# Kernel optimization log

Hardware: AMD Instinct MI355X
Metric: run time of the kernel (lower is better)

Reference implementation:

```python
import jax, jax.numpy as jnp
import numpy as np

D_DYN = 256    # dynamic_dim
D_STAT = 64    # static_dim
U_DIM = 48     # config.model.u_dim
N_OBS = 80     # num_prod*2 + num_inj = 32*2 + 16
T = 128        # rollout steps
B = 2048       # batch


def setup_inputs() -> dict:
    key = jax.random.key(0)
    k = jax.random.split(key, 8)
    z_dyn = jax.random.normal(k[0], (B, D_DYN), dtype=jnp.float32)
    z_static = jax.random.normal(k[1], (B, D_STAT), dtype=jnp.float32)
    dt = jnp.ones((1,), dtype=jnp.float32) * 0.05
    U = jax.random.normal(k[2], (T, B, U_DIM), dtype=jnp.float32)
    # learned params, initialized as in the torch module
    eig_raw = jnp.zeros((D_DYN,), dtype=jnp.float32)
    V = jnp.eye(D_DYN, dtype=jnp.float32) + jax.random.normal(k[3], (D_DYN, D_DYN), dtype=jnp.float32) * 0.01
    L = jax.random.normal(k[4], (D_DYN, U_DIM), dtype=jnp.float32) * (1.0 / np.sqrt(U_DIM))
    C = jax.random.normal(k[5], (N_OBS, D_DYN), dtype=jnp.float32) * (1.0 / np.sqrt(D_DYN))
    Dm = jax.random.normal(k[6], (N_OBS, U_DIM), dtype=jnp.float32) * (1.0 / np.sqrt(U_DIM))
    return {"z_dyn": z_dyn, "z_static": z_static, "dt": dt, "U": U,
            "eig_raw": eig_raw, "V": V, "L": L, "C": C, "Dm": Dm}


def reference(z_dyn, z_static, dt, U, eig_raw, V, L, C, Dm):
    # Stable Koopman operator: K = V diag(sigmoid(eig_raw)*0.99) V^{-1}
    eigvals = jax.nn.sigmoid(eig_raw) * 0.99
    K = (V * eigvals[None, :]) @ jnp.linalg.inv(V)  # [d, d]
    KT, LT, CT, DT = K.T, L.T, C.T, Dm.T
    dts = dt[0]

    def step(z, ut):
        ut_dt = ut * dts                 # [B, u_dim]
        z = z @ KT + ut_dt @ LT          # [B, d]
        y = z @ CT + ut_dt @ DT          # [B, n_obs]
        return z, (z, y)

    _, (Z, Y) = jax.lax.scan(step, z_dyn, U)
    return Z, Y  # [T, B, d], [T, B, n_obs]
```

## Files before the change

kernel.cpp:

```cpp
#include <hip/hip_runtime.h>

#define D_   256
#define UD_  48
#define NO_  80
#define T_   128
#define B_   2048

typedef __bf16 bf16x8 __attribute__((ext_vector_type(8)));
typedef float  f32x4  __attribute__((ext_vector_type(4)));
typedef unsigned short ushort_t;

static __device__ __forceinline__ ushort_t f2bf(float f){
  return __builtin_bit_cast(ushort_t, (__bf16)f);
}
static __device__ __forceinline__ float bf2f(ushort_t u){
  union { unsigned int i; float f; } c; c.i = ((unsigned int)u) << 16; return c.f;
}
static __device__ __forceinline__ f32x4 mfma16(bf16x8 a, bf16x8 b, f32x4 c){
  return __builtin_amdgcn_mfma_f32_16x16x32_bf16(a, b, c, 0, 0, 0);
}


__global__ void __launch_bounds__(256) k_pre(
    const float* __restrict__ V, const float* __restrict__ eig,
    const float* __restrict__ Cmat,
    float* __restrict__ W, float* __restrict__ Cw,
    float* __restrict__ lam, float* __restrict__ dVd){
  const int bid = blockIdx.x, tid = threadIdx.x;
  if (bid < 256){
    const float* Ar = V + bid*D_;
    float a0=0.f,a1=0.f,a2=0.f,a3=0.f;
    #pragma unroll 4
    for (int k = 0; k < D_; k += 4){
      a0 += Ar[k+0] * V[(k+0)*D_ + tid];
      a1 += Ar[k+1] * V[(k+1)*D_ + tid];
      a2 += Ar[k+2] * V[(k+2)*D_ + tid];
      a3 += Ar[k+3] * V[(k+3)*D_ + tid];
    }
    W[bid*D_ + tid] = (a0+a1)+(a2+a3);
  } else if (bid < 256 + NO_){
    const int n = bid - 256;
    float acc = 0.f;
    #pragma unroll 4
    for (int j = 0; j < D_; ++j) acc += Cmat[n*D_ + j] * V[j*D_ + tid];
    Cw[n*D_ + tid] = acc;
  } else {
    lam[tid] = 0.99f / (1.0f + expf(-eig[tid]));
    const float v = V[tid*D_ + tid];
    dVd[tid] = v - bf2f(f2bf(v));
  }
}

__global__ void __launch_bounds__(256) k_x1(
    const float* __restrict__ V, const float* __restrict__ W,
    float* __restrict__ X1){
  const int i = blockIdx.x, j = threadIdx.x;
  const float* Ar = V + i*D_;
  float a0=0.f,a1=0.f,a2=0.f,a3=0.f;
  #pragma unroll 4
  for (int k = 0; k < D_; k += 4){
    a0 += Ar[k+0] * W[(k+0)*D_ + j];
    a1 += Ar[k+1] * W[(k+1)*D_ + j];
    a2 += Ar[k+2] * W[(k+2)*D_ + j];
    a3 += Ar[k+3] * W[(k+3)*D_ + j];
  }
  X1[i*D_ + j] = (i == j ? 4.0f : 0.0f) - 6.0f*V[i*D_ + j] + 4.0f*W[i*D_ + j]
                 - ((a0+a1)+(a2+a3));
}

__global__ void __launch_bounds__(256) k_mm_mul(
    const float* __restrict__ A, const float* __restrict__ B,
    float* __restrict__ Cm){
  const int i = blockIdx.x, j = threadIdx.x;
  const float* Ar = A + i*D_;
  float a0=0.f,a1=0.f,a2=0.f,a3=0.f;
  #pragma unroll 4
  for (int k = 0; k < D_; k += 4){
    a0 += Ar[k+0] * B[(k+0)*D_ + j];
    a1 += Ar[k+1] * B[(k+1)*D_ + j];
    a2 += Ar[k+2] * B[(k+2)*D_ + j];
    a3 += Ar[k+3] * B[(k+3)*D_ + j];
  }
  Cm[i*D_ + j] = (a0+a1)+(a2+a3);
}

__global__ void __launch_bounds__(256) k_x2(
    const float* __restrict__ X1, const float* __restrict__ Tm,
    const float* __restrict__ Lmat, const float* __restrict__ dt,
    float* __restrict__ VinvT, float* __restrict__ Lw){
  __shared__ float row[256];
  const int i = blockIdx.x, j = threadIdx.x;
  const float* Xr = X1 + i*D_;
  float a0=0.f,a1=0.f,a2=0.f,a3=0.f;
  #pragma unroll 4
  for (int k = 0; k < D_; k += 4){
    a0 += Xr[k+0] * Tm[(k+0)*D_ + j];
    a1 += Xr[k+1] * Tm[(k+1)*D_ + j];
    a2 += Xr[k+2] * Tm[(k+2)*D_ + j];
    a3 += Xr[k+3] * Tm[(k+3)*D_ + j];
  }
  const float out = 2.0f*Xr[j] - ((a0+a1)+(a2+a3));
  VinvT[j*D_ + i] = out;
  row[j] = out;
  __syncthreads();
  if (j < UD_){
    float acc = 0.f;
    #pragma unroll 4
    for (int k = 0; k < D_; ++k) acc += row[k] * Lmat[k*UD_ + j];
    Lw[i*UD_ + j] = acc * dt[0];
  }
}

__global__ void __launch_bounds__(256) k_prep2(
    const float* __restrict__ z0, const float* __restrict__ VinvT,
    const float* __restrict__ Lw, const float* __restrict__ V,
    const float* __restrict__ Cw, const float* __restrict__ Dmat,
    const float* __restrict__ dt,
    ushort_t* __restrict__ Wchk, ushort_t* __restrict__ Lws,
    ushort_t* __restrict__ Af){
  __shared__ float zr[8][256];
  const int bid = blockIdx.x, tid = threadIdx.x;
  if (bid < 256){
    const int b0 = bid * 8;
    #pragma unroll
    for (int r = 0; r < 8; ++r) zr[r][tid] = z0[(size_t)(b0+r)*D_ + tid];
    __syncthreads();
    float acc[8] = {0.f,0.f,0.f,0.f,0.f,0.f,0.f,0.f};
    #pragma unroll 4
    for (int j = 0; j < D_; ++j){
      const float vj = VinvT[j*D_ + tid];
      #pragma unroll
      for (int r = 0; r < 8; ++r) acc[r] += zr[r][j] * vj;
    }
    #pragma unroll
    for (int r = 0; r < 8; ++r)
      Wchk[(size_t)(b0+r)*D_ + tid] = f2bf(acc[r]);
  } else if (bid < 288){
    const int f = bid - 256;
    if (tid < 64){
      const int l = tid, lm = l & 15, lh = l >> 4;
      const int it = f >> 1, kc2 = f & 1;
      const int ig = it*16 + lm;
      #pragma unroll
      for (int j = 0; j < 8; ++j){
        const int k = 32*kc2 + 4*lh + (j & 3) + 16*(j >> 2);
        Lws[(f*64 + l)*8 + j] = f2bf(k < UD_ ? Lw[ig*UD_ + k] : 0.f);
      }
    }
  } else {
    const int v = (bid - 288)*4 + (tid >> 6);
    if (v < 210){
      const int mt = v / 10, kc = v % 10;
      const int l = tid & 63, lm = l & 15, lh = l >> 4;
      const float dts = dt[0];
      #pragma unroll
      for (int j = 0; j < 8; ++j){
        const int k = 32*kc + 4*lh + (j & 3) + 16*(j >> 2);
        float val = 0.f;
        if (mt < 16){
          if (kc < 8) val = V[(mt*16 + lm)*D_ + k];
        } else {
          const int n = (mt - 16)*16 + lm;
          if (kc < 8) val = Cw[n*D_ + k];
          else { const int ku = k - 256; if (ku < UD_) val = dts * Dmat[n*UD_ + ku]; }
        }
        Af[((size_t)(mt*10 + kc)*64 + l)*8 + j] = f2bf(val);
      }
    }
  }
}


#define LSCAN_STEP(UA, UB, UC) do {                                             \
  union { ushort_t us[8]; bf16x8 v; } c0, c1;                                   \
  c0.us[0]=f2bf((UA).x); c0.us[1]=f2bf((UA).y); c0.us[2]=f2bf((UA).z); c0.us[3]=f2bf((UA).w); \
  c0.us[4]=f2bf((UB).x); c0.us[5]=f2bf((UB).y); c0.us[6]=f2bf((UB).z); c0.us[7]=f2bf((UB).w); \
  c1.us[0]=f2bf((UC).x); c1.us[1]=f2bf((UC).y); c1.us[2]=f2bf((UC).z); c1.us[3]=f2bf((UC).w); \
  c1.us[4]=0; c1.us[5]=0; c1.us[6]=0; c1.us[7]=0;                               \
  _Pragma("unroll")                                                             \
  for (int q = 0; q < 4; ++q){                                                  \
    f32x4 acc = {0.f,0.f,0.f,0.f};                                              \
    acc = mfma16(lwf[q*2+0], c0.v, acc);                                        \
    acc = mfma16(lwf[q*2+1], c1.v, acc);                                        \
    _Pragma("unroll")                                                           \
    for (int r = 0; r < 4; ++r) w[q*4+r] = lamr[q*4+r]*w[q*4+r] + acc[r];       \
  }                                                                             \
} while(0)

__global__ void __launch_bounds__(256) k_scanA(const float* __restrict__ U,
    const ushort_t* __restrict__ Lws, const float* __restrict__ lam,
    ushort_t* __restrict__ Wchk){
  const int tid = threadIdx.x;
  const int wid = tid >> 6, l = tid & 63;
  const int lm = l & 15, lh = l >> 4;
  const int ch = blockIdx.x >> 7;
  const int bq = blockIdx.x & 127;
  const int row = bq*16 + lm;
  const int itb = wid*4;

  bf16x8 lwf[8];
  #pragma unroll
  for (int q = 0; q < 4; ++q)
    #pragma unroll
    for (int c = 0; c < 2; ++c)
      lwf[q*2 + c] = *(const bf16x8*)(Lws + ((size_t)(((itb+q)*2 + c)*64 + l))*8);

  float lamr[16], w[16];
  #pragma unroll
  for (int q = 0; q < 4; ++q){
    const int i = (itb+q)*16 + 4*lh;
    const float4 lv = *(const float4*)&lam[i];
    lamr[q*4+0]=lv.x; lamr[q*4+1]=lv.y; lamr[q*4+2]=lv.z; lamr[q*4+3]=lv.w;
    w[q*4+0]=0.f; w[q*4+1]=0.f; w[q*4+2]=0.f; w[q*4+3]=0.f;
  }

  const size_t TS = (size_t)B_ * UD_;
  const float* Urow = U + ((size_t)(ch*8)*B_ + row) * UD_;
  float4 Aa, Ab, Ac, Ba, Bb, Bc;
  Aa = *(const float4*)&Urow[4*lh]; Ab = *(const float4*)&Urow[16+4*lh]; Ac = *(const float4*)&Urow[32+4*lh];
  { const float* Up = Urow + TS;
    Ba = *(const float4*)&Up[4*lh]; Bb = *(const float4*)&Up[16+4*lh]; Bc = *(const float4*)&Up[32+4*lh]; }

  #pragma unroll
  for (int tt = 0; tt < 4; ++tt){
    LSCAN_STEP(Aa, Ab, Ac);
    if (tt < 3){
      const float* Up = Urow + (size_t)(2*tt+2)*TS;
      Aa = *(const float4*)&Up[4*lh]; Ab = *(const float4*)&Up[16+4*lh]; Ac = *(const float4*)&Up[32+4*lh];
    }
    LSCAN_STEP(Ba, Bb, Bc);
    if (tt < 3){
      const float* Up = Urow + (size_t)(2*tt+3)*TS;
      Ba = *(const float4*)&Up[4*lh]; Bb = *(const float4*)&Up[16+4*lh]; Bc = *(const float4*)&Up[32+4*lh];
    }
  }
  #pragma unroll
  for (int q = 0; q < 4; ++q){
    const int i = (itb+q)*16 + 4*lh;
    ushort4 o; o.x=f2bf(w[q*4+0]); o.y=f2bf(w[q*4+1]); o.z=f2bf(w[q*4+2]); o.w=f2bf(w[q*4+3]);
    *(ushort4*)(Wchk + ((size_t)(ch+1)*B_ + row)*D_ + i) = o;
  }
}

__global__ void __launch_bounds__(256) k_scanB(const float* __restrict__ lam,
    ushort_t* __restrict__ Wchk){
  const int d = threadIdx.x;
  const int b0 = blockIdx.x * 16;
  float l2 = lam[d]; l2 = l2*l2;
  float l8 = l2*l2;  l8 = l8*l8;
  float W[16];
  #pragma unroll
  for (int r = 0; r < 16; ++r)
    W[r] = bf2f(Wchk[(size_t)(b0+r)*D_ + d]);
  #pragma unroll 1
  for (int j = 0; j < 15; ++j){
    ushort_t* slot = Wchk + (size_t)(j+1)*B_*D_;
    #pragma unroll
    for (int r = 0; r < 16; ++r){
      const float c = bf2f(slot[(size_t)(b0+r)*D_ + d]);
      W[r] = l8*W[r] + c;
      slot[(size_t)(b0+r)*D_ + d] = f2bf(W[r]);
    }
  }
}

__global__ void __launch_bounds__(256) k_fused(
    const float* __restrict__ U, const ushort_t* __restrict__ Af,
    const ushort_t* __restrict__ Lws, const float* __restrict__ lam,
    const float* __restrict__ dVd, const ushort_t* __restrict__ Wchk,
    float* __restrict__ outZ, float* __restrict__ outY){
  __shared__ __align__(16) ushort_t AfZhL[8*8*512];
  __shared__ __align__(16) ushort_t LwsL[32*512];
  __shared__ __align__(16) ushort_t AfYhL[40*512];
  __shared__ __align__(16) float    trbZ[4][16][68];
  __shared__ __align__(16) float    dVdL[128];
  __shared__ __align__(16) float    lamL[256];

  const int tid = threadIdx.x;
  const int bid = blockIdx.x;
  const int h  = bid & 1;
  const int ch = (bid >> 1) & 15;
  const int bq = bid >> 5;
  const int wid = tid >> 6, l = tid & 63;
  const int lm = l & 15, lh = l >> 4;
  const int col0 = bq*64 + wid*16;
  const int col = col0 + lm;

  {
    const uint4* gsrc = (const uint4*)Af;
    uint4* dz = (uint4*)AfZhL;
    #pragma unroll
    for (int r = 0; r < 16; ++r){
      const int i = r*256 + tid;
      const int f = i >> 6, l4 = i & 63;
      const int mi8 = f >> 3, kc = f & 7;
      dz[i] = gsrc[(size_t)((h*8 + mi8)*10 + kc)*64 + l4];
    }
    uint4* dy = (uint4*)AfYhL;
    const int nY = h ? 640 : 2560;
    const int sb = 16 + (h ? 4 : 0);
    #pragma unroll
    for (int r = 0; r < 10; ++r){
      const int i = r*256 + tid;
      if (i < nY){
        const int f = i >> 6, l4 = i & 63;
        const int myl = f / 10, j = f % 10;
        dy[i] = gsrc[(size_t)((sb + myl)*10 + j)*64 + l4];
      }
    }
    const uint4* ls = (const uint4*)Lws;
    uint4* ld = (uint4*)LwsL;
    #pragma unroll
    for (int r = 0; r < 8; ++r) ld[r*256 + tid] = ls[r*256 + tid];
    if (tid < 32) ((float4*)dVdL)[tid] = ((const float4*)(dVd + h*128))[tid];
    else if (tid < 96) ((float4*)lamL)[tid-32] = ((const float4*)lam)[tid-32];
  }

  float w[64];
  #pragma unroll
  for (int kc = 0; kc < 8; ++kc)
    #pragma unroll
    for (int hh = 0; hh < 2; ++hh){
      const int i = 32*kc + 16*hh + 4*lh;
      const ushort4 wu = *(const ushort4*)(Wchk + ((size_t)ch*B_ + col)*D_ + i);
      const int e = 8*kc + 4*hh;
      w[e+0]=bf2f(wu.x); w[e+1]=bf2f(wu.y); w[e+2]=bf2f(wu.z); w[e+3]=bf2f(wu.w);
    }

  const size_t TS = (size_t)B_ * UD_;
  const float* Ucol = U + (size_t)col * UD_;
  float4 ua, ub, uc;
  {
    const float* Ut = Ucol + (size_t)(ch*8)*TS;
    ua = *(const float4*)&Ut[4*lh]; ub = *(const float4*)&Ut[16+4*lh]; uc = *(const float4*)&Ut[32+4*lh];
  }

  __syncthreads();

#define ZLOOP(HH)                                                               \
  { float* zbase = outZ + ((size_t)t*B_ + col0)*D_ + (HH)*128;                  \
    _Pragma("unroll")                                                           \
    for (int g = 0; g < 2; ++g){                                                \
      _Pragma("unroll")                                                         \
      for (int mi = 0; mi < 4; ++mi){                                           \
        const int mi8 = g*4 + mi;                                               \
        f32x4 acc = {0.f,0.f,0.f,0.f};                                          \
        _Pragma("unroll")                                                       \
        for (int kc = 0; kc < 8; ++kc){                                         \
          const bf16x8 af = *(const bf16x8*)&AfZhL[((mi8*8+kc)*64 + l)*8];      \
          acc = mfma16(af, wfr[kc], acc);                                       \
        }                                                                       \
        const float4 dv = *(const float4*)&dVdL[mi8*16 + 4*lh];                 \
        acc[0] += dv.x * (float)wfr[((HH)*8+mi8)>>1][0 + 4*(mi8&1)];            \
        acc[1] += dv.y * (float)wfr[((HH)*8+mi8)>>1][1 + 4*(mi8&1)];            \
        acc[2] += dv.z * (float)wfr[((HH)*8+mi8)>>1][2 + 4*(mi8&1)];            \
        acc[3] += dv.w * (float)wfr[((HH)*8+mi8)>>1][3 + 4*(mi8&1)];            \
        *(float4*)&trbZ[wid][lm][mi*16 + 4*lh] = make_float4(acc[0],acc[1],acc[2],acc[3]); \
      }                                                                         \
      __builtin_amdgcn_wave_barrier();                                          \
      _Pragma("unroll")                                                         \
      for (int j = 0; j < 4; ++j){                                              \
        const int r_ = j*4 + (l >> 4), c16 = l & 15;                            \
        const float4 v = *(const float4*)&trbZ[wid][r_][4*c16];                 \
        *(float4*)&zbase[(size_t)r_*D_ + g*64 + 4*c16] = v;                     \
      }                                                                         \
      __builtin_amdgcn_wave_barrier();                                          \
    } }

#define YLOOP(COFF, NMY)                                                        \
  { float* yrow = outY + ((size_t)t*B_ + col)*NO_ + (COFF);                     \
    _Pragma("unroll")                                                           \
    for (int my = 0; my < (NMY); ++my){                                         \
      f32x4 acc = {0.f,0.f,0.f,0.f};                                            \
      _Pragma("unroll")                                                         \
      for (int kc = 0; kc < 8; ++kc){                                           \
        const bf16x8 af = *(const bf16x8*)&AfYhL[((my*10+kc)*64 + l)*8];        \
        acc = mfma16(af, wfr[kc], acc);                                         \
      }                                                                         \
      { const bf16x8 af8 = *(const bf16x8*)&AfYhL[((my*10+8)*64 + l)*8];        \
        const bf16x8 af9 = *(const bf16x8*)&AfYhL[((my*10+9)*64 + l)*8];        \
        acc = mfma16(af8, uf0, acc); acc = mfma16(af9, uf1, acc); }             \
      *(float4*)&yrow[my*16 + 4*lh] = make_float4(acc[0],acc[1],acc[2],acc[3]); \
    } }

  #pragma unroll 1
  for (int s = 0; s < 8; ++s){
    const int t = ch*8 + s;
    bf16x8 uf0, uf1;
    {
      union { ushort_t us[8]; bf16x8 v; } cv;
      cv.us[0]=f2bf(ua.x); cv.us[1]=f2bf(ua.y); cv.us[2]=f2bf(ua.z); cv.us[3]=f2bf(ua.w);
      cv.us[4]=f2bf(ub.x); cv.us[5]=f2bf(ub.y); cv.us[6]=f2bf(ub.z); cv.us[7]=f2bf(ub.w);
      uf0 = cv.v;
      cv.us[0]=f2bf(uc.x); cv.us[1]=f2bf(uc.y); cv.us[2]=f2bf(uc.z); cv.us[3]=f2bf(uc.w);
      cv.us[4]=0; cv.us[5]=0; cv.us[6]=0; cv.us[7]=0;
      uf1 = cv.v;
    }
    if (s < 7){
      const float* Ut = Ucol + (size_t)(t+1)*TS;
      ua = *(const float4*)&Ut[4*lh]; ub = *(const float4*)&Ut[16+4*lh]; uc = *(const float4*)&Ut[32+4*lh];
    }
    #pragma unroll
    for (int it = 0; it < 16; ++it){
      const bf16x8 a0 = *(const bf16x8*)&LwsL[((it*2+0)*64 + l)*8];
      const bf16x8 a1 = *(const bf16x8*)&LwsL[((it*2+1)*64 + l)*8];
      const float4 lv = *(const float4*)&lamL[32*(it>>1) + 16*(it&1) + 4*lh];
      f32x4 acc = {0.f,0.f,0.f,0.f};
      acc = mfma16(a0, uf0, acc);
      acc = mfma16(a1, uf1, acc);
      const int e0 = 8*(it>>1) + 4*(it&1);
      w[e0+0] = lv.x*w[e0+0] + acc[0];
      w[e0+1] = lv.y*w[e0+1] + acc[1];
      w[e0+2] = lv.z*w[e0+2] + acc[2];
      w[e0+3] = lv.w*w[e0+3] + acc[3];
    }
    bf16x8 wfr[8];
    #pragma unroll
    for (int kc = 0; kc < 8; ++kc){
      union { ushort_t us[8]; bf16x8 v; } cv;
      #pragma unroll
      for (int j = 0; j < 8; ++j) cv.us[j] = f2bf(w[8*kc + j]);
      wfr[kc] = cv.v;
    }
    if (h == 0){
      ZLOOP(0);
      YLOOP(0, 4);
    } else {
      ZLOOP(1);
      YLOOP(64, 1);
    }
  }
#undef ZLOOP
#undef YLOOP
}

extern "C" void kernel_launch(void* const* d_in, const int* in_sizes, int n_in,
                              void* d_out, int out_size, void* d_ws, size_t ws_size,
                              hipStream_t stream){
  const float* z0  = (const float*)d_in[0];
  const float* dt  = (const float*)d_in[2];
  const float* U   = (const float*)d_in[3];
  const float* eig = (const float*)d_in[4];
  const float* V   = (const float*)d_in[5];
  const float* L   = (const float*)d_in[6];
  const float* C   = (const float*)d_in[7];
  const float* Dm  = (const float*)d_in[8];
  float* outZ = (float*)d_out;
  float* outY = outZ + (size_t)T_*B_*D_;

  char* ws = (char*)d_ws;
  float* Xa    = (float*)(ws + 0);
  float* Xb    = (float*)(ws + 262144);
  float* Tt    = (float*)(ws + 524288);
  float* Lw    = (float*)(ws + 786432);
  float* Cw    = (float*)(ws + 835584);
  float* lam   = (float*)(ws + 917504);
  float* dVd   = (float*)(ws + 918528);
  ushort_t* Af   = (ushort_t*)(ws + 919552);
  ushort_t* Lws  = (ushort_t*)(ws + 1134592);
  ushort_t* Wchk = (ushort_t*)(ws + 1167360);
  if (ws_size < 17944576u) return;

  k_pre   <<<337,256,0,stream>>>(V, eig, C, Xa, Cw, lam, dVd);
  k_x1    <<<256,256,0,stream>>>(V, Xa, Xb);
  k_mm_mul<<<256,256,0,stream>>>(V, Xb, Tt);
  k_x2    <<<256,256,0,stream>>>(Xb, Tt, L, dt, Xa, Lw);
  k_prep2 <<<342,256,0,stream>>>(z0, Xa, Lw, V, Cw, Dm, dt, Wchk, Lws, Af);
  k_scanA <<<1920,256,0,stream>>>(U, Lws, lam, Wchk);
  k_scanB <<<128,256,0,stream>>>(lam, Wchk);
  k_fused <<<1024,256,0,stream>>>(U, Af, Lws, lam, dVd, Wchk, outZ, outY);
}
```

Measured before the change: 262.0 us.

## Restructure inverse polynomial, drop scanB carry kernel, fold prefix into fused kernel

The Newton-Schulz style inverse is re-expressed as a polynomial in V using V^2, V^3 and V^4, computed in one batched kernel. That removes one serial matmul launch from the setup chain. The separate chunk-carry kernel k_scanB is removed, and each k_fused block now combines the earlier chunk partials with lambda^8 itself before rolling out. This trades an extra launch and a serial pass for redundant per-block work that grows with the chunk index. An s_setprio hint is also added around the MFMA and store loop.

Measured after the change: 403.0 us. 53.8% more time.

```diff
diff --git a/kernel.cpp b/kernel.cpp
--- a/kernel.cpp
+++ b/kernel.cpp
@@ -21,7 +21,7 @@
 }
 
 
-__global__ void __launch_bounds__(256) k_pre(
+__global__ void __launch_bounds__(256) k1(
     const float* __restrict__ V, const float* __restrict__ eig,
     const float* __restrict__ Cmat,
     float* __restrict__ W, float* __restrict__ Cw,
@@ -51,55 +51,43 @@
   }
 }
 
-__global__ void __launch_bounds__(256) k_x1(
+__global__ void __launch_bounds__(256) k2(
     const float* __restrict__ V, const float* __restrict__ W,
-    float* __restrict__ X1){
-  const int i = blockIdx.x, j = threadIdx.x;
-  const float* Ar = V + i*D_;
+    float* __restrict__ V3, float* __restrict__ V4){
+  const int bid = blockIdx.x, tid = threadIdx.x;
+  const int i = bid & 255;
+  const float* Ar = (bid < 256 ? V : W) + i*D_;
   float a0=0.f,a1=0.f,a2=0.f,a3=0.f;
   #pragma unroll 4
   for (int k = 0; k < D_; k += 4){
-    a0 += Ar[k+0] * W[(k+0)*D_ + j];
-    a1 += Ar[k+1] * W[(k+1)*D_ + j];
-    a2 += Ar[k+2] * W[(k+2)*D_ + j];
-    a3 += Ar[k+3] * W[(k+3)*D_ + j];
-  }
-  X1[i*D_ + j] = (i == j ? 4.0f : 0.0f) - 6.0f*V[i*D_ + j] + 4.0f*W[i*D_ + j]
-                 - ((a0+a1)+(a2+a3));
-}
-
-__global__ void __launch_bounds__(256) k_mm_mul(
-    const float* __restrict__ A, const float* __restrict__ B,
-    float* __restrict__ Cm){
-  const int i = blockIdx.x, j = threadIdx.x;
-  const float* Ar = A + i*D_;
-  float a0=0.f,a1=0.f,a2=0.f,a3=0.f;
-  #pragma unroll 4
-  for (int k = 0; k < D_; k += 4){
-    a0 += Ar[k+0] * B[(k+0)*D_ + j];
-    a1 += Ar[k+1] * B[(k+1)*D_ + j];
-    a2 += Ar[k+2] * B[(k+2)*D_ + j];
-    a3 += Ar[k+3] * B[(k+3)*D_ + j];
-  }
-  Cm[i*D_ + j] = (a0+a1)+(a2+a3);
-}
-
-__global__ void __launch_bounds__(256) k_x2(
-    const float* __restrict__ X1, const float* __restrict__ Tm,
+    a0 += Ar[k+0] * W[(k+0)*D_ + tid];
+    a1 += Ar[k+1] * W[(k+1)*D_ + tid];
+    a2 += Ar[k+2] * W[(k+2)*D_ + tid];
+    a3 += Ar[k+3] * W[(k+3)*D_ + tid];
+  }
+  float* dst = (bid < 256) ? V3 : V4;
+  dst[i*D_ + tid] = (a0+a1)+(a2+a3);
+}
+
+__global__ void __launch_bounds__(256) k3(
+    const float* __restrict__ V, const float* __restrict__ W,
+    const float* __restrict__ V3, const float* __restrict__ V4,
     const float* __restrict__ Lmat, const float* __restrict__ dt,
     float* __restrict__ VinvT, float* __restrict__ Lw){
   __shared__ float row[256];
   const int i = blockIdx.x, j = threadIdx.x;
-  const float* Xr = X1 + i*D_;
+  const float* r4 = V4 + i*D_;
   float a0=0.f,a1=0.f,a2=0.f,a3=0.f;
   #pragma unroll 4
   for (int k = 0; k < D_; k += 4){
-    a0 += Xr[k+0] * Tm[(k+0)*D_ + j];
-    a1 += Xr[k+1] * Tm[(k+1)*D_ + j];
-    a2 += Xr[k+2] * Tm[(k+2)*D_ + j];
-    a3 += Xr[k+3] * Tm[(k+3)*D_ + j];
-  }
-  const float out = 2.0f*Xr[j] - ((a0+a1)+(a2+a3));
+    a0 += r4[k+0] * (-28.f*V[(k+0)*D_+j] + 8.f*W[(k+0)*D_+j] - V3[(k+0)*D_+j]);
+    a1 += r4[k+1] * (-28.f*V[(k+1)*D_+j] + 8.f*W[(k+1)*D_+j] - V3[(k+1)*D_+j]);
+    a2 += r4[k+2] * (-28.f*V[(k+2)*D_+j] + 8.f*W[(k+2)*D_+j] - V3[(k+2)*D_+j]);
+    a3 += r4[k+3] * (-28.f*V[(k+3)*D_+j] + 8.f*W[(k+3)*D_+j] - V3[(k+3)*D_+j]);
+  }
+  const float out = (i == j ? 8.f : 0.f)
+                  - 28.f*V[i*D_+j] + 56.f*W[i*D_+j] - 70.f*V3[i*D_+j] + 56.f*V4[i*D_+j]
+                  + ((a0+a1)+(a2+a3));
   VinvT[j*D_ + i] = out;
   row[j] = out;
   __syncthreads();
@@ -169,7 +157,6 @@
     }
   }
 }
-
 
 #define LSCAN_STEP(UA, UB, UC) do {                                             \
   union { ushort_t us[8]; bf16x8 v; } c0, c1;                                   \
@@ -242,28 +229,6 @@
   }
 }
 
-__global__ void __launch_bounds__(256) k_scanB(const float* __restrict__ lam,
-    ushort_t* __restrict__ Wchk){
-  const int d = threadIdx.x;
-  const int b0 = blockIdx.x * 16;
-  float l2 = lam[d]; l2 = l2*l2;
-  float l8 = l2*l2;  l8 = l8*l8;
-  float W[16];
-  #pragma unroll
-  for (int r = 0; r < 16; ++r)
-    W[r] = bf2f(Wchk[(size_t)(b0+r)*D_ + d]);
-  #pragma unroll 1
-  for (int j = 0; j < 15; ++j){
-    ushort_t* slot = Wchk + (size_t)(j+1)*B_*D_;
-    #pragma unroll
-    for (int r = 0; r < 16; ++r){
-      const float c = bf2f(slot[(size_t)(b0+r)*D_ + d]);
-      W[r] = l8*W[r] + c;
-      slot[(size_t)(b0+r)*D_ + d] = f2bf(W[r]);
-    }
-  }
-}
-
 __global__ void __launch_bounds__(256) k_fused(
     const float* __restrict__ U, const ushort_t* __restrict__ Af,
     const ushort_t* __restrict__ Lws, const float* __restrict__ lam,
@@ -322,7 +287,7 @@
     #pragma unroll
     for (int hh = 0; hh < 2; ++hh){
       const int i = 32*kc + 16*hh + 4*lh;
-      const ushort4 wu = *(const ushort4*)(Wchk + ((size_t)ch*B_ + col)*D_ + i);
+      const ushort4 wu = *(const ushort4*)(Wchk + (size_t)col*D_ + i);
       const int e = 8*kc + 4*hh;
       w[e+0]=bf2f(wu.x); w[e+1]=bf2f(wu.y); w[e+2]=bf2f(wu.z); w[e+3]=bf2f(wu.w);
     }
@@ -336,6 +301,39 @@
   }
 
   __syncthreads();
+
+  if (ch > 0){
+    float l8v[64];
+    #pragma unroll
+    for (int kc = 0; kc < 8; ++kc)
+      #pragma unroll
+      for (int hh = 0; hh < 2; ++hh){
+        const int i = 32*kc + 16*hh + 4*lh;
+        const float4 lv = *(const float4*)&lamL[i];
+        const int e = 8*kc + 4*hh;
+        float t;
+        t = lv.x; t = t*t; t = t*t; t = t*t; l8v[e+0] = t;
+        t = lv.y; t = t*t; t = t*t; t = t*t; l8v[e+1] = t;
+        t = lv.z; t = t*t; t = t*t; t = t*t; l8v[e+2] = t;
+        t = lv.w; t = t*t; t = t*t; t = t*t; l8v[e+3] = t;
+      }
+    #pragma unroll 1
+    for (int j = 1; j <= ch; ++j){
+      const ushort_t* slot = Wchk + (size_t)j*B_*D_ + (size_t)col*D_;
+      #pragma unroll
+      for (int kc = 0; kc < 8; ++kc)
+        #pragma unroll
+        for (int hh = 0; hh < 2; ++hh){
+          const int i = 32*kc + 16*hh + 4*lh;
+          const ushort4 cu = *(const ushort4*)(slot + i);
+          const int e = 8*kc + 4*hh;
+          w[e+0] = l8v[e+0]*w[e+0] + bf2f(cu.x);
+          w[e+1] = l8v[e+1]*w[e+1] + bf2f(cu.y);
+          w[e+2] = l8v[e+2]*w[e+2] + bf2f(cu.z);
+          w[e+3] = l8v[e+3]*w[e+3] + bf2f(cu.w);
+        }
+    }
+  }
 
 #define ZLOOP(HH)                                                               \
   { float* zbase = outZ + ((size_t)t*B_ + col0)*D_ + (HH)*128;                  \
@@ -400,6 +398,7 @@
       const float* Ut = Ucol + (size_t)(t+1)*TS;
       ua = *(const float4*)&Ut[4*lh]; ub = *(const float4*)&Ut[16+4*lh]; uc = *(const float4*)&Ut[32+4*lh];
     }
+    __builtin_amdgcn_s_setprio(1);
     #pragma unroll
     for (int it = 0; it < 16; ++it){
       const bf16x8 a0 = *(const bf16x8*)&LwsL[((it*2+0)*64 + l)*8];
@@ -429,6 +428,7 @@
       ZLOOP(1);
       YLOOP(64, 1);
     }
+    __builtin_amdgcn_s_setprio(0);
   }
 #undef ZLOOP
 #undef YLOOP
@@ -449,9 +449,9 @@
   float* outY = outZ + (size_t)T_*B_*D_;
 
   char* ws = (char*)d_ws;
-  float* Xa    = (float*)(ws + 0);
-  float* Xb    = (float*)(ws + 262144);
-  float* Tt    = (float*)(ws + 524288);
+  float* Wm    = (float*)(ws + 0);
+  float* V3m   = (float*)(ws + 262144);
+  float* VinvT = (float*)(ws + 524288);
   float* Lw    = (float*)(ws + 786432);
   float* Cw    = (float*)(ws + 835584);
   float* lam   = (float*)(ws + 917504);
@@ -459,14 +459,13 @@
   ushort_t* Af   = (ushort_t*)(ws + 919552);
   ushort_t* Lws  = (ushort_t*)(ws + 1134592);
   ushort_t* Wchk = (ushort_t*)(ws + 1167360);
+  float* V4m   = (float*)(ws + 1167360 + (size_t)B_*D_*2);
   if (ws_size < 17944576u) return;
 
-  k_pre   <<<337,256,0,stream>>>(V, eig, C, Xa, Cw, lam, dVd);
-  k_x1    <<<256,256,0,stream>>>(V, Xa, Xb);
-  k_mm_mul<<<256,256,0,stream>>>(V, Xb, Tt);
-  k_x2    <<<256,256,0,stream>>>(Xb, Tt, L, dt, Xa, Lw);
-  k_prep2 <<<342,256,0,stream>>>(z0, Xa, Lw, V, Cw, Dm, dt, Wchk, Lws, Af);
-  k_scanA <<<1920,256,0,stream>>>(U, Lws, lam, Wchk);
-  k_scanB <<<128,256,0,stream>>>(lam, Wchk);
-  k_fused <<<1024,256,0,stream>>>(U, Af, Lws, lam, dVd, Wchk, outZ, outY);
-}
+  k1     <<<337,256,0,stream>>>(V, eig, C, Wm, Cw, lam, dVd);
+  k2     <<<512,256,0,stream>>>(V, Wm, V3m, V4m);
+  k3     <<<256,256,0,stream>>>(V, Wm, V3m, V4m, L, dt, VinvT, Lw);
+  k_prep2<<<342,256,0,stream>>>(z0, VinvT, Lw, V, Cw, Dm, dt, Wchk, Lws, Af);
+  k_scanA<<<1920,256,0,stream>>>(U, Lws, lam, Wchk);
+  k_fused<<<1024,256,0,stream>>>(U, Af, Lws, lam, dVd, Wchk, outZ, outY);
+}
```
